# Performance work log

Measured on AMD Instinct MI355X. Metric: run time of the kernel, lower is better.

## Reference

```python
import jax, jax.numpy as jnp
import numpy as np

MARGIN = 1.0  # config['margin']


def setup_inputs() -> dict:
    key = jax.random.key(0)
    k1, k2 = jax.random.split(key)
    features = jax.random.normal(k1, (1024, 512), dtype=jnp.float32)
    labels = jax.random.randint(k2, (1024,), 0, 32)
    return {"features": features, "labels": labels}


def _cdist(x):
    # Pairwise euclidean distances, matching torch.cdist; zero-distance
    # entries (e.g., the diagonal) get zero gradient like torch's backward.
    sq = jnp.sum(x * x, axis=-1)
    d2 = sq[:, None] + sq[None, :] - 2.0 * (x @ x.T)
    d2 = jnp.maximum(d2, 0.0)
    safe = jnp.where(d2 > 0.0, d2, 1.0)
    return jnp.where(d2 > 0.0, jnp.sqrt(safe), 0.0)


def reference(features, labels):
    n = features.shape[0]
    dist = _cdist(features)                                   # [N, N]
    pos = (labels[:, None] == labels[None, :]).astype(features.dtype)  # includes diagonal, as in the torch code
    neg = 1.0 - pos

    # loss = sum_i sum_{p in pos(i)} sum_{k in neg(i)} relu(d[i,p] - d[i,k] + margin)
    # Stream over anchors i to avoid materializing the [N, N, N] broadcast.
    def per_anchor(args):
        di, pi, ni = args  # each [N]
        t = jax.nn.relu(di[:, None] - di[None, :] + MARGIN)   # [N_pos_axis, N_neg_axis]
        return jnp.sum(t * (pi[:, None] * ni[None, :]))

    losses = jax.lax.map(per_anchor, (dist, pos, neg))        # [N]
    return jnp.sum(losses) / (n + 1e-8)
```

## Files before the change

### kernel.cpp

```cpp
#include <hip/hip_runtime.h>
#include <math.h>

#define MARGIN 1.0f
#define N_MAX 1024
#define BK 64

typedef short short8 __attribute__((ext_vector_type(8)));
typedef unsigned short ushort8 __attribute__((ext_vector_type(8)));
typedef float floatx16 __attribute__((ext_vector_type(16)));

__device__ inline unsigned short bf16_rne(float x) {
  unsigned u = __float_as_uint(x);
  unsigned r = (u + 0x7FFF + ((u >> 16) & 1)) >> 16;
  return (unsigned short)r;
}
__device__ inline float bf16_to_f32(unsigned short h) {
  return __uint_as_float(((unsigned)h) << 16);
}

__global__ __launch_bounds__(64) void conv_kernel(
    const float* __restrict__ f, unsigned short* __restrict__ fhi,
    unsigned short* __restrict__ flo, float* __restrict__ sq, int N, int D) {
  const int r = blockIdx.x;
  const int t = threadIdx.x;
  float acc = 0.f;
  if (t * 8 < D) {
    const float* src = f + (size_t)r * D + t * 8;
    float4 v0 = *(const float4*)(src);
    float4 v1 = *(const float4*)(src + 4);
    float xs[8] = {v0.x, v0.y, v0.z, v0.w, v1.x, v1.y, v1.z, v1.w};
    ushort8 hs, ls;
#pragma unroll
    for (int e = 0; e < 8; ++e) {
      float x = xs[e];
      acc += x * x;
      unsigned short h = bf16_rne(x);
      hs[e] = h;
      ls[e] = bf16_rne(x - bf16_to_f32(h));
    }
    const size_t off = ((size_t)t * N + r) * 8;
    *(ushort8*)(fhi + off) = hs;
    *(ushort8*)(flo + off) = ls;
  }
  for (int off = 32; off > 0; off >>= 1) acc += __shfl_down(acc, off, 64);
  if (t == 0) sq[r] = acc;
}

__global__ __launch_bounds__(256) void dist_kernel(
    const unsigned short* __restrict__ fhi, const unsigned short* __restrict__ flo,
    const float* __restrict__ sqv, float* __restrict__ dist, int N, int D) {
  __shared__ ushort8 T[2][4][8][64];

  const int tid = threadIdx.x;
  const int w = tid >> 6;
  const int lane = tid & 63;
  const int rowBase = blockIdx.y * 64;
  const int colBase = blockIdx.x * 64;

  const unsigned short* srcs[4] = {fhi, flo, fhi, flo};
  const int bases[4] = {rowBase, rowBase, colBase, colBase};

  const int wr = (w >> 1) * 32;
  const int wc = (w & 1) * 32;
  const int m = lane & 31;
  const int h = lane >> 5;

  ushort8 regs[8];

  auto loadRegs = [&](int k0) {
    const int c0 = k0 >> 3;
#pragma unroll
    for (int s = 0; s < 8; ++s) {
      const int a = s >> 1;
      const int c = (w << 1) | (s & 1);
      regs[s] = *(const ushort8*)(srcs[a] + ((size_t)(c0 + c) * N + bases[a] + lane) * 8);
    }
  };
  auto storeRegs = [&](int b) {
#pragma unroll
    for (int s = 0; s < 8; ++s) {
      const int a = s >> 1;
      const int c = (w << 1) | (s & 1);
      T[b][a][c][lane] = regs[s];
    }
  };

  floatx16 acc = {};
  int b = 0;

  loadRegs(0);
  storeRegs(0);

  for (int k0 = 0; k0 < D; k0 += BK) {
    if (k0 + BK < D) loadRegs(k0 + BK);
    __syncthreads();
#pragma unroll
    for (int kk = 0; kk < BK / 16; ++kk) {
      const int c = 2 * kk + h;
      short8 ahf = *(const short8*)&T[b][0][c][wr + m];
      short8 alf = *(const short8*)&T[b][1][c][wr + m];
      short8 bhf = *(const short8*)&T[b][2][c][wc + m];
      short8 blf = *(const short8*)&T[b][3][c][wc + m];
      acc = __builtin_amdgcn_mfma_f32_32x32x16_bf16(ahf, bhf, acc, 0, 0, 0);
      acc = __builtin_amdgcn_mfma_f32_32x32x16_bf16(ahf, blf, acc, 0, 0, 0);
      acc = __builtin_amdgcn_mfma_f32_32x32x16_bf16(alf, bhf, acc, 0, 0, 0);
    }
    if (k0 + BK < D) storeRegs(b ^ 1);
    b ^= 1;
  }

  const int col = colBase + wc + m;
  const float sqc = sqv[col];
#pragma unroll
  for (int r = 0; r < 16; ++r) {
    const int row = rowBase + wr + (r & 3) + 8 * (r >> 2) + 4 * h;
    float d2 = sqv[row] + sqc - 2.0f * acc[r];
    d2 = d2 > 0.f ? d2 : 0.f;
    dist[(size_t)row * N + col] = sqrtf(d2);
  }
}

__global__ __launch_bounds__(256) void anchor_loss_kernel(
    const float* __restrict__ dist, const int* __restrict__ labels,
    float* __restrict__ partial, int N) {
  const int i = blockIdx.x;
  const int tid = threadIdx.x;
  const int lane = tid & 63;

  __shared__ float dpos[N_MAX];
  __shared__ float dneg[N_MAX];
  __shared__ int cnt[2];
  __shared__ float red[4];

  if (tid < 2) cnt[tid] = 0;
  __syncthreads();

  const int lab = labels[i];
  const float* drow = dist + (size_t)i * N;

  for (int jb = 0; jb < N; jb += 256) {
    int j = jb + tid;
    bool valid = j < N;
    float d = valid ? drow[j] : 0.f;
    bool isPos = valid && (labels[j & (N_MAX - 1)] == lab);
    bool isNeg = valid && !isPos;

    unsigned long long mp = __ballot(isPos);
    unsigned long long mn = __ballot(isNeg);
    unsigned long long lt = (1ull << lane) - 1ull;

    int base_p = 0, base_n = 0;
    if (lane == 0) {
      base_p = atomicAdd(&cnt[0], __popcll(mp));
      base_n = atomicAdd(&cnt[1], __popcll(mn));
    }
    base_p = __shfl(base_p, 0, 64);
    base_n = __shfl(base_n, 0, 64);

    if (isPos) dpos[base_p + __popcll(mp & lt)] = d + MARGIN;
    if (isNeg) dneg[base_n + __popcll(mn & lt)] = d;
  }
  __syncthreads();

  const int np = cnt[0], nn = cnt[1];

  float dk[4];
#pragma unroll
  for (int e = 0; e < 4; ++e) {
    int k = tid + 256 * e;
    dk[e] = (k < nn) ? dneg[k] : 1e30f;
  }

  float accv = 0.f;
  for (int p = 0; p < np; ++p) {
    float t = dpos[p];
#pragma unroll
    for (int e = 0; e < 4; ++e) {
      float v = t - dk[e];
      accv += (v > 0.f) ? v : 0.f;
    }
  }

  for (int off = 32; off > 0; off >>= 1) accv += __shfl_down(accv, off, 64);
  if (lane == 0) red[tid >> 6] = accv;
  __syncthreads();
  if (tid == 0) partial[i] = red[0] + red[1] + red[2] + red[3];
}

__global__ __launch_bounds__(256) void final_reduce_kernel(
    const float* __restrict__ partial, float* __restrict__ out, int N) {
  float acc = 0.f;
  for (int j = threadIdx.x; j < N; j += 256) acc += partial[j];
  for (int off = 32; off > 0; off >>= 1) acc += __shfl_down(acc, off, 64);
  __shared__ float red[4];
  if ((threadIdx.x & 63) == 0) red[threadIdx.x >> 6] = acc;
  __syncthreads();
  if (threadIdx.x == 0) {
    double s = (double)red[0] + (double)red[1] + (double)red[2] + (double)red[3];
    out[0] = (float)(s / ((double)N + 1e-8));
  }
}

extern "C" void kernel_launch(void* const* d_in, const int* in_sizes, int n_in,
                              void* d_out, int out_size, void* d_ws, size_t ws_size,
                              hipStream_t stream) {
  const float* f = (const float*)d_in[0];
  const int* labels = (const int*)d_in[1];
  int N = in_sizes[1];
  int D = in_sizes[0] / N;
  float* out = (float*)d_out;

  unsigned short* fhi = (unsigned short*)d_ws;
  unsigned short* flo = fhi + (size_t)N * D;
  float* sq = (float*)(flo + (size_t)N * D);
  float* dist = sq + N;
  float* partial = dist + (size_t)N * N;

  conv_kernel<<<N, 64, 0, stream>>>(f, fhi, flo, sq, N, D);
  dim3 grid(N / 64, N / 64);
  dist_kernel<<<grid, 256, 0, stream>>>(fhi, flo, sq, dist, N, D);
  anchor_loss_kernel<<<N, 256, 0, stream>>>(dist, labels, partial, N);
  final_reduce_kernel<<<1, 256, 0, stream>>>(partial, out, N);
}
```

Measured before the change: 78.67 us.

## Fuse conversion, distance GEMM and triplet loss into one cooperative kernel

```diff
diff --git a/kernel.cpp b/kernel.cpp
--- a/kernel.cpp
+++ b/kernel.cpp
@@ -1,9 +1,10 @@
 #include <hip/hip_runtime.h>
+#include <hip/hip_cooperative_groups.h>
 #include <math.h>
 
+namespace cg = cooperative_groups;
+
 #define MARGIN 1.0f
-#define N_MAX 1024
-#define BK 64
 
 typedef short short8 __attribute__((ext_vector_type(8)));
 typedef unsigned short ushort8 __attribute__((ext_vector_type(8)));
@@ -18,186 +19,167 @@
   return __uint_as_float(((unsigned)h) << 16);
 }
 
-__global__ __launch_bounds__(64) void conv_kernel(
-    const float* __restrict__ f, unsigned short* __restrict__ fhi,
-    unsigned short* __restrict__ flo, float* __restrict__ sq, int N, int D) {
-  const int r = blockIdx.x;
-  const int t = threadIdx.x;
-  float acc = 0.f;
-  if (t * 8 < D) {
-    const float* src = f + (size_t)r * D + t * 8;
-    float4 v0 = *(const float4*)(src);
-    float4 v1 = *(const float4*)(src + 4);
-    float xs[8] = {v0.x, v0.y, v0.z, v0.w, v1.x, v1.y, v1.z, v1.w};
-    ushort8 hs, ls;
-#pragma unroll
-    for (int e = 0; e < 8; ++e) {
-      float x = xs[e];
-      acc += x * x;
-      unsigned short h = bf16_rne(x);
-      hs[e] = h;
-      ls[e] = bf16_rne(x - bf16_to_f32(h));
-    }
-    const size_t off = ((size_t)t * N + r) * 8;
-    *(ushort8*)(fhi + off) = hs;
-    *(ushort8*)(flo + off) = ls;
+__global__ __launch_bounds__(256, 2) void mega_kernel(
+    const float* __restrict__ f, const int* __restrict__ labels,
+    unsigned short* __restrict__ fhi, unsigned short* __restrict__ flo,
+    float* __restrict__ sq, float* dist, float* gacc, int* ticket,
+    float* __restrict__ out, int N, int D) {
+  __shared__ ushort8 T[2][4][8][64];
+
+  cg::grid_group grid = cg::this_grid();
+  const int tid = threadIdx.x;
+  const int bid = blockIdx.x;
+  const int lane = tid & 63;
+  const int w = tid >> 6;
+
+  {
+    if (bid == 0 && tid == 0) { *gacc = 0.f; *ticket = 0; }
+    const int row = bid * 4 + w;
+    const int c = lane;
+    float a = 0.f;
+    if (c * 8 < D) {
+      const float* src = f + (size_t)row * D + c * 8;
+      float4 v0 = *(const float4*)(src);
+      float4 v1 = *(const float4*)(src + 4);
+      float xs[8] = {v0.x, v0.y, v0.z, v0.w, v1.x, v1.y, v1.z, v1.w};
+      ushort8 hs, ls;
+#pragma unroll
+      for (int e = 0; e < 8; ++e) {
+        float x = xs[e];
+        a += x * x;
+        unsigned short hh = bf16_rne(x);
+        hs[e] = hh;
+        ls[e] = bf16_rne(x - bf16_to_f32(hh));
+      }
+      const size_t off = ((size_t)c * N + row) * 8;
+      *(ushort8*)(fhi + off) = hs;
+      *(ushort8*)(flo + off) = ls;
+    }
+    for (int o = 32; o > 0; o >>= 1) a += __shfl_down(a, o, 64);
+    if (lane == 0) sq[row] = a;
   }
-  for (int off = 32; off > 0; off >>= 1) acc += __shfl_down(acc, off, 64);
-  if (t == 0) sq[r] = acc;
-}
-
-__global__ __launch_bounds__(256) void dist_kernel(
-    const unsigned short* __restrict__ fhi, const unsigned short* __restrict__ flo,
-    const float* __restrict__ sqv, float* __restrict__ dist, int N, int D) {
-  __shared__ ushort8 T[2][4][8][64];
-
-  const int tid = threadIdx.x;
-  const int w = tid >> 6;
-  const int lane = tid & 63;
-  const int rowBase = blockIdx.y * 64;
-  const int colBase = blockIdx.x * 64;
-
-  const unsigned short* srcs[4] = {fhi, flo, fhi, flo};
-  const int bases[4] = {rowBase, rowBase, colBase, colBase};
-
-  const int wr = (w >> 1) * 32;
-  const int wc = (w & 1) * 32;
-  const int m = lane & 31;
-  const int h = lane >> 5;
-
-  ushort8 regs[8];
-
-  auto loadRegs = [&](int k0) {
-    const int c0 = k0 >> 3;
-#pragma unroll
-    for (int s = 0; s < 8; ++s) {
-      const int a = s >> 1;
-      const int c = (w << 1) | (s & 1);
-      regs[s] = *(const ushort8*)(srcs[a] + ((size_t)(c0 + c) * N + bases[a] + lane) * 8);
-    }
-  };
-  auto storeRegs = [&](int b) {
-#pragma unroll
-    for (int s = 0; s < 8; ++s) {
-      const int a = s >> 1;
-      const int c = (w << 1) | (s & 1);
-      T[b][a][c][lane] = regs[s];
-    }
-  };
-
-  floatx16 acc = {};
-  int b = 0;
-
-  loadRegs(0);
-  storeRegs(0);
-
-  for (int k0 = 0; k0 < D; k0 += BK) {
-    if (k0 + BK < D) loadRegs(k0 + BK);
+  __threadfence();
+  grid.sync();
+
+  {
+    const int by = bid >> 4, bx = bid & 15;
+    const int rowBase = by * 64, colBase = bx * 64;
+    const unsigned short* srcs[4] = {fhi, flo, fhi, flo};
+    const int bases[4] = {rowBase, rowBase, colBase, colBase};
+    const int wr = (w >> 1) * 32;
+    const int wc = (w & 1) * 32;
+    const int m = lane & 31;
+    const int h = lane >> 5;
+
+    ushort8 regs[8];
+    auto loadRegs = [&](int k0) {
+      const int c0 = k0 >> 3;
+#pragma unroll
+      for (int s = 0; s < 8; ++s) {
+        const int a = s >> 1;
+        const int c = (w << 1) | (s & 1);
+        regs[s] = *(const ushort8*)(srcs[a] + ((size_t)(c0 + c) * N + bases[a] + lane) * 8);
+      }
+    };
+    auto storeRegs = [&](int b) {
+#pragma unroll
+      for (int s = 0; s < 8; ++s) {
+        const int a = s >> 1;
+        const int c = (w << 1) | (s & 1);
+        T[b][a][c][lane] = regs[s];
+      }
+    };
+
+    floatx16 acc = {};
+    int b = 0;
+    loadRegs(0);
+    storeRegs(0);
+    for (int k0 = 0; k0 < D; k0 += 64) {
+      if (k0 + 64 < D) loadRegs(k0 + 64);
+      __syncthreads();
+#pragma unroll
+      for (int kk = 0; kk < 4; ++kk) {
+        const int c = 2 * kk + h;
+        short8 ahf = *(const short8*)&T[b][0][c][wr + m];
+        short8 alf = *(const short8*)&T[b][1][c][wr + m];
+        short8 bhf = *(const short8*)&T[b][2][c][wc + m];
+        short8 blf = *(const short8*)&T[b][3][c][wc + m];
+        acc = __builtin_amdgcn_mfma_f32_32x32x16_bf16(ahf, bhf, acc, 0, 0, 0);
+        acc = __builtin_amdgcn_mfma_f32_32x32x16_bf16(ahf, blf, acc, 0, 0, 0);
+        acc = __builtin_amdgcn_mfma_f32_32x32x16_bf16(alf, bhf, acc, 0, 0, 0);
+      }
+      if (k0 + 64 < D) storeRegs(b ^ 1);
+      b ^= 1;
+    }
+
+    const int col = colBase + wc + m;
+    const float sqc = sq[col];
+#pragma unroll
+    for (int r = 0; r < 16; ++r) {
+      const int row = rowBase + wr + (r & 3) + 8 * (r >> 2) + 4 * h;
+      float d2 = sq[row] + sqc - 2.0f * acc[r];
+      d2 = d2 > 0.f ? d2 : 0.f;
+      dist[(size_t)row * N + col] = sqrtf(d2);
+    }
+  }
+  __threadfence();
+  grid.sync();
+
+  {
     __syncthreads();
-#pragma unroll
-    for (int kk = 0; kk < BK / 16; ++kk) {
-      const int c = 2 * kk + h;
-      short8 ahf = *(const short8*)&T[b][0][c][wr + m];
-      short8 alf = *(const short8*)&T[b][1][c][wr + m];
-      short8 bhf = *(const short8*)&T[b][2][c][wc + m];
-      short8 blf = *(const short8*)&T[b][3][c][wc + m];
-      acc = __builtin_amdgcn_mfma_f32_32x32x16_bf16(ahf, bhf, acc, 0, 0, 0);
-      acc = __builtin_amdgcn_mfma_f32_32x32x16_bf16(ahf, blf, acc, 0, 0, 0);
-      acc = __builtin_amdgcn_mfma_f32_32x32x16_bf16(alf, bhf, acc, 0, 0, 0);
-    }
-    if (k0 + BK < D) storeRegs(b ^ 1);
-    b ^= 1;
-  }
-
-  const int col = colBase + wc + m;
-  const float sqc = sqv[col];
-#pragma unroll
-  for (int r = 0; r < 16; ++r) {
-    const int row = rowBase + wr + (r & 3) + 8 * (r >> 2) + 4 * h;
-    float d2 = sqv[row] + sqc - 2.0f * acc[r];
-    d2 = d2 > 0.f ? d2 : 0.f;
-    dist[(size_t)row * N + col] = sqrtf(d2);
-  }
-}
-
-__global__ __launch_bounds__(256) void anchor_loss_kernel(
-    const float* __restrict__ dist, const int* __restrict__ labels,
-    float* __restrict__ partial, int N) {
-  const int i = blockIdx.x;
-  const int tid = threadIdx.x;
-  const int lane = tid & 63;
-
-  __shared__ float dpos[N_MAX];
-  __shared__ float dneg[N_MAX];
-  __shared__ int cnt[2];
-  __shared__ float red[4];
-
-  if (tid < 2) cnt[tid] = 0;
-  __syncthreads();
-
-  const int lab = labels[i];
-  const float* drow = dist + (size_t)i * N;
-
-  for (int jb = 0; jb < N; jb += 256) {
-    int j = jb + tid;
-    bool valid = j < N;
-    float d = valid ? drow[j] : 0.f;
-    bool isPos = valid && (labels[j & (N_MAX - 1)] == lab);
-    bool isNeg = valid && !isPos;
-
-    unsigned long long mp = __ballot(isPos);
-    unsigned long long mn = __ballot(isNeg);
-    unsigned long long lt = (1ull << lane) - 1ull;
-
-    int base_p = 0, base_n = 0;
-    if (lane == 0) {
-      base_p = atomicAdd(&cnt[0], __popcll(mp));
-      base_n = atomicAdd(&cnt[1], __popcll(mn));
-    }
-    base_p = __shfl(base_p, 0, 64);
-    base_n = __shfl(base_n, 0, 64);
-
-    if (isPos) dpos[base_p + __popcll(mp & lt)] = d + MARGIN;
-    if (isNeg) dneg[base_n + __popcll(mn & lt)] = d;
-  }
-  __syncthreads();
-
-  const int np = cnt[0], nn = cnt[1];
-
-  float dk[4];
-#pragma unroll
-  for (int e = 0; e < 4; ++e) {
-    int k = tid + 256 * e;
-    dk[e] = (k < nn) ? dneg[k] : 1e30f;
-  }
-
-  float accv = 0.f;
-  for (int p = 0; p < np; ++p) {
-    float t = dpos[p];
-#pragma unroll
-    for (int e = 0; e < 4; ++e) {
-      float v = t - dk[e];
-      accv += (v > 0.f) ? v : 0.f;
-    }
-  }
-
-  for (int off = 32; off > 0; off >>= 1) accv += __shfl_down(accv, off, 64);
-  if (lane == 0) red[tid >> 6] = accv;
-  __syncthreads();
-  if (tid == 0) partial[i] = red[0] + red[1] + red[2] + red[3];
-}
-
-__global__ __launch_bounds__(256) void final_reduce_kernel(
-    const float* __restrict__ partial, float* __restrict__ out, int N) {
-  float acc = 0.f;
-  for (int j = threadIdx.x; j < N; j += 256) acc += partial[j];
-  for (int off = 32; off > 0; off >>= 1) acc += __shfl_down(acc, off, 64);
-  __shared__ float red[4];
-  if ((threadIdx.x & 63) == 0) red[threadIdx.x >> 6] = acc;
-  __syncthreads();
-  if (threadIdx.x == 0) {
-    double s = (double)red[0] + (double)red[1] + (double)red[2] + (double)red[3];
-    out[0] = (float)(s / ((double)N + 1e-8));
+    float* buf = ((float*)T) + w * 1056;
+    const int i = bid * 4 + w;
+    const int lab = labels[i];
+    const float* drow = dist + (size_t)i * N;
+
+    int cp = 0, cn = 0;
+    for (int it = 0; it < 16; ++it) {
+      int j = it * 64 + lane;
+      float d = drow[j];
+      bool isPos = (labels[j] == lab);
+      unsigned long long mp = __ballot(isPos);
+      unsigned long long lt = (1ull << lane) - 1ull;
+      int pp = __popcll(mp & lt);
+      if (isPos) buf[cp + pp] = d;
+      else       buf[1023 - cn - (lane - pp)] = d;
+      int npos = __popcll(mp);
+      cp += npos;
+      cn += 64 - npos;
+    }
+    __syncthreads();
+
+    const int np = cp, nn = cn;
+    float dk[16];
+#pragma unroll
+    for (int e = 0; e < 16; ++e) {
+      int k = e * 64 + lane;
+      dk[e] = (k < nn) ? buf[1023 - k] : 1e30f;
+    }
+
+    float accv = 0.f;
+    for (int p = 0; p < np; ++p) {
+      float t = buf[p] + MARGIN;
+#pragma unroll
+      for (int e = 0; e < 16; ++e) {
+        float v = t - dk[e];
+        accv += (v > 0.f) ? v : 0.f;
+      }
+    }
+
+    for (int o = 32; o > 0; o >>= 1) accv += __shfl_down(accv, o, 64);
+    float* red = ((float*)T) + 4 * 1056;
+    if (lane == 0) red[w] = accv;
+    __syncthreads();
+    if (tid == 0) {
+      float bsum = red[0] + red[1] + red[2] + red[3];
+      atomicAdd(gacc, bsum);
+      __threadfence();
+      int old = atomicAdd(ticket, 1);
+      if (old == (int)gridDim.x - 1) {
+        float total = atomicAdd(gacc, 0.0f);
+        out[0] = (float)((double)total / ((double)N + 1e-8));
+      }
+    }
   }
 }
 
@@ -214,11 +196,9 @@
   unsigned short* flo = fhi + (size_t)N * D;
   float* sq = (float*)(flo + (size_t)N * D);
   float* dist = sq + N;
-  float* partial = dist + (size_t)N * N;
-
-  conv_kernel<<<N, 64, 0, stream>>>(f, fhi, flo, sq, N, D);
-  dim3 grid(N / 64, N / 64);
-  dist_kernel<<<grid, 256, 0, stream>>>(fhi, flo, sq, dist, N, D);
-  anchor_loss_kernel<<<N, 256, 0, stream>>>(dist, labels, partial, N);
-  final_reduce_kernel<<<1, 256, 0, stream>>>(partial, out, N);
-}
+  float* gacc = dist + (size_t)N * N;
+  int* ticket = (int*)(gacc + 1);
+
+  void* args[] = {&f, &labels, &fhi, &flo, &sq, &dist, &gacc, &ticket, &out, &N, &D};
+  hipLaunchCooperativeKernel((void*)mega_kernel, dim3(256), dim3(256), args, 0, stream);
+}
```

After: 211.1 us. +168.4%, slower.

## Fuse bf16 hi/lo split and norm computation into distance GEMM kernel

Applied to the files above, without the earlier changes.

```diff
diff --git a/kernel.cpp b/kernel.cpp
--- a/kernel.cpp
+++ b/kernel.cpp
@@ -2,8 +2,6 @@
 #include <math.h>
 
 #define MARGIN 1.0f
-#define N_MAX 1024
-#define BK 64
 
 typedef short short8 __attribute__((ext_vector_type(8)));
 typedef unsigned short ushort8 __attribute__((ext_vector_type(8)));
@@ -18,37 +16,8 @@
   return __uint_as_float(((unsigned)h) << 16);
 }
 
-__global__ __launch_bounds__(64) void conv_kernel(
-    const float* __restrict__ f, unsigned short* __restrict__ fhi,
-    unsigned short* __restrict__ flo, float* __restrict__ sq, int N, int D) {
-  const int r = blockIdx.x;
-  const int t = threadIdx.x;
-  float acc = 0.f;
-  if (t * 8 < D) {
-    const float* src = f + (size_t)r * D + t * 8;
-    float4 v0 = *(const float4*)(src);
-    float4 v1 = *(const float4*)(src + 4);
-    float xs[8] = {v0.x, v0.y, v0.z, v0.w, v1.x, v1.y, v1.z, v1.w};
-    ushort8 hs, ls;
-#pragma unroll
-    for (int e = 0; e < 8; ++e) {
-      float x = xs[e];
-      acc += x * x;
-      unsigned short h = bf16_rne(x);
-      hs[e] = h;
-      ls[e] = bf16_rne(x - bf16_to_f32(h));
-    }
-    const size_t off = ((size_t)t * N + r) * 8;
-    *(ushort8*)(fhi + off) = hs;
-    *(ushort8*)(flo + off) = ls;
-  }
-  for (int off = 32; off > 0; off >>= 1) acc += __shfl_down(acc, off, 64);
-  if (t == 0) sq[r] = acc;
-}
-
-__global__ __launch_bounds__(256) void dist_kernel(
-    const unsigned short* __restrict__ fhi, const unsigned short* __restrict__ flo,
-    const float* __restrict__ sqv, float* __restrict__ dist, int N, int D) {
+__global__ __launch_bounds__(256) void dist_fused_kernel(
+    const float* __restrict__ f, float* __restrict__ dist, int N, int D) {
   __shared__ ushort8 T[2][4][8][64];
 
   const int tid = threadIdx.x;
@@ -57,45 +26,60 @@
   const int rowBase = blockIdx.y * 64;
   const int colBase = blockIdx.x * 64;
 
-  const unsigned short* srcs[4] = {fhi, flo, fhi, flo};
-  const int bases[4] = {rowBase, rowBase, colBase, colBase};
+  const int sr = tid & 63;
+  const int q = tid >> 6;
 
   const int wr = (w >> 1) * 32;
   const int wc = (w & 1) * 32;
   const int m = lane & 31;
   const int h = lane >> 5;
 
-  ushort8 regs[8];
-
-  auto loadRegs = [&](int k0) {
-    const int c0 = k0 >> 3;
-#pragma unroll
-    for (int s = 0; s < 8; ++s) {
-      const int a = s >> 1;
-      const int c = (w << 1) | (s & 1);
-      regs[s] = *(const ushort8*)(srcs[a] + ((size_t)(c0 + c) * N + bases[a] + lane) * 8);
+  float aF[16], bF[16];
+  float asq_part = 0.f, bsq_part = 0.f;
+
+  auto loadF = [&](int k0) {
+    const float* pa = f + (size_t)(rowBase + sr) * D + k0 + q * 16;
+    const float* pb = f + (size_t)(colBase + sr) * D + k0 + q * 16;
+#pragma unroll
+    for (int v = 0; v < 4; ++v) {
+      *(float4*)&aF[4 * v] = *(const float4*)(pa + 4 * v);
+      *(float4*)&bF[4 * v] = *(const float4*)(pb + 4 * v);
     }
   };
-  auto storeRegs = [&](int b) {
-#pragma unroll
-    for (int s = 0; s < 8; ++s) {
-      const int a = s >> 1;
-      const int c = (w << 1) | (s & 1);
-      T[b][a][c][lane] = regs[s];
+  auto convStore = [&](int b) {
+#pragma unroll
+    for (int half = 0; half < 2; ++half) {
+      ushort8 ah, al, bh, bl;
+#pragma unroll
+      for (int e = 0; e < 8; ++e) {
+        float xa = aF[half * 8 + e];
+        float xb = bF[half * 8 + e];
+        asq_part += xa * xa;
+        bsq_part += xb * xb;
+        unsigned short hA = bf16_rne(xa);
+        unsigned short hB = bf16_rne(xb);
+        ah[e] = hA; al[e] = bf16_rne(xa - bf16_to_f32(hA));
+        bh[e] = hB; bl[e] = bf16_rne(xb - bf16_to_f32(hB));
+      }
+      const int c = 2 * q + half;
+      T[b][0][c][sr] = ah;
+      T[b][1][c][sr] = al;
+      T[b][2][c][sr] = bh;
+      T[b][3][c][sr] = bl;
     }
   };
 
   floatx16 acc = {};
   int b = 0;
 
-  loadRegs(0);
-  storeRegs(0);
-
-  for (int k0 = 0; k0 < D; k0 += BK) {
-    if (k0 + BK < D) loadRegs(k0 + BK);
+  loadF(0);
+  convStore(0);
+
+  for (int k0 = 0; k0 < D; k0 += 64) {
+    if (k0 + 64 < D) loadF(k0 + 64);
     __syncthreads();
 #pragma unroll
-    for (int kk = 0; kk < BK / 16; ++kk) {
+    for (int kk = 0; kk < 4; ++kk) {
       const int c = 2 * kk + h;
       short8 ahf = *(const short8*)&T[b][0][c][wr + m];
       short8 alf = *(const short8*)&T[b][1][c][wr + m];
@@ -105,18 +89,26 @@
       acc = __builtin_amdgcn_mfma_f32_32x32x16_bf16(ahf, blf, acc, 0, 0, 0);
       acc = __builtin_amdgcn_mfma_f32_32x32x16_bf16(alf, bhf, acc, 0, 0, 0);
     }
-    if (k0 + BK < D) storeRegs(b ^ 1);
+    if (k0 + 64 < D) convStore(b ^ 1);
     b ^= 1;
   }
 
-  const int col = colBase + wc + m;
-  const float sqc = sqv[col];
+  __syncthreads();
+  float* sqbuf = (float*)T;
+  sqbuf[q * 64 + sr] = asq_part;
+  sqbuf[256 + q * 64 + sr] = bsq_part;
+  __syncthreads();
+
+  const int colL = wc + m;
+  const float sqc = sqbuf[256 + colL] + sqbuf[320 + colL] + sqbuf[384 + colL] + sqbuf[448 + colL];
+  const int col = colBase + colL;
 #pragma unroll
   for (int r = 0; r < 16; ++r) {
-    const int row = rowBase + wr + (r & 3) + 8 * (r >> 2) + 4 * h;
-    float d2 = sqv[row] + sqc - 2.0f * acc[r];
+    const int rowL = wr + (r & 3) + 8 * (r >> 2) + 4 * h;
+    const float sqr = sqbuf[rowL] + sqbuf[64 + rowL] + sqbuf[128 + rowL] + sqbuf[192 + rowL];
+    float d2 = sqr + sqc - 2.0f * acc[r];
     d2 = d2 > 0.f ? d2 : 0.f;
-    dist[(size_t)row * N + col] = sqrtf(d2);
+    dist[(size_t)(rowBase + rowL) * N + col] = sqrtf(d2);
   }
 }
 
@@ -127,8 +119,8 @@
   const int tid = threadIdx.x;
   const int lane = tid & 63;
 
-  __shared__ float dpos[N_MAX];
-  __shared__ float dneg[N_MAX];
+  __shared__ float dpos[1024];
+  __shared__ float dneg[1024];
   __shared__ int cnt[2];
   __shared__ float red[4];
 
@@ -140,25 +132,23 @@
 
   for (int jb = 0; jb < N; jb += 256) {
     int j = jb + tid;
-    bool valid = j < N;
-    float d = valid ? drow[j] : 0.f;
-    bool isPos = valid && (labels[j & (N_MAX - 1)] == lab);
-    bool isNeg = valid && !isPos;
+    float d = drow[j];
+    bool isPos = (labels[j] == lab);
 
     unsigned long long mp = __ballot(isPos);
-    unsigned long long mn = __ballot(isNeg);
+    unsigned long long mn = ~mp;
     unsigned long long lt = (1ull << lane) - 1ull;
 
     int base_p = 0, base_n = 0;
     if (lane == 0) {
       base_p = atomicAdd(&cnt[0], __popcll(mp));
-      base_n = atomicAdd(&cnt[1], __popcll(mn));
+      base_n = atomicAdd(&cnt[1], 64 - __popcll(mp));
     }
     base_p = __shfl(base_p, 0, 64);
     base_n = __shfl(base_n, 0, 64);
 
     if (isPos) dpos[base_p + __popcll(mp & lt)] = d + MARGIN;
-    if (isNeg) dneg[base_n + __popcll(mn & lt)] = d;
+    else       dneg[base_n + __popcll(mn & lt)] = d;
   }
   __syncthreads();
 
@@ -210,15 +200,11 @@
   int D = in_sizes[0] / N;
   float* out = (float*)d_out;
 
-  unsigned short* fhi = (unsigned short*)d_ws;
-  unsigned short* flo = fhi + (size_t)N * D;
-  float* sq = (float*)(flo + (size_t)N * D);
-  float* dist = sq + N;
+  float* dist = (float*)d_ws;
   float* partial = dist + (size_t)N * N;
 
-  conv_kernel<<<N, 64, 0, stream>>>(f, fhi, flo, sq, N, D);
   dim3 grid(N / 64, N / 64);
-  dist_kernel<<<grid, 256, 0, stream>>>(fhi, flo, sq, dist, N, D);
+  dist_fused_kernel<<<grid, 256, 0, stream>>>(f, dist, N, D);
   anchor_loss_kernel<<<N, 256, 0, stream>>>(dist, labels, partial, N);
   final_reduce_kernel<<<1, 256, 0, stream>>>(partial, out, N);
 }
```

After: 83.12 us. +5.7%, slower.
